# Kernel tuning notes

Hardware: AMD Instinct MI355X
Metric: run time of the kernel (lower is better)

## Reference

```python
import jax, jax.numpy as jnp
import numpy as np

B, S, F = 64, 512, 64
H, L = 512, 4
NH = 8
DH = H // NH
ALPHA = 0.1
EPS = 1e-5


def setup_inputs() -> dict:
    key = jax.random.key(0)
    ks = iter(jax.random.split(key, 40))
    def g(shape, scale=0.05):
        return jax.random.normal(next(ks), shape, dtype=jnp.float32) * scale
    z = lambda *shape: jnp.zeros(shape, dtype=jnp.float32)
    inp = {
        'x': jax.random.normal(next(ks), (B, S, F), dtype=jnp.float32),
        # top-level input projection
        'Win0': g((H, F)), 'bin0': z(H),
        # stacked LTC layer params (L, ...)
        'Wi': g((L, H, H)), 'bi': z(L, H),
        'Wh': g((L, H, H)), 'bh': z(L, H),
        'Wo': g((L, H, H)), 'bo': z(L, H),
        'ln_g': jnp.ones((L, H), dtype=jnp.float32), 'ln_b': z(L, H),
        # multihead self-attention (torch nn.MultiheadAttention packed qkv)
        'in_proj_w': g((3 * H, H)), 'in_proj_b': z(3 * H),
        'out_w': g((H, H)), 'out_b': z(H),
        # direction head
        'Wd1': g((H // 2, H)), 'bd1': z(H // 2),
        'Wd2': g((H // 4, H // 2)), 'bd2': z(H // 4),
        'Wd3': g((2, H // 4)), 'bd3': z(2),
        # price head
        'Wq1': g((H // 2, H)), 'bq1': z(H // 2),
        'Wq2': g((H // 4, H // 2)), 'bq2': z(H // 4),
        'Wq3': g((1, H // 4)), 'bq3': z(1),
        # confidence head
        'Wc1': g((H // 2, H)), 'bc1': z(H // 2),
        'Wc2': g((1, H // 2)), 'bc2': z(1),
    }
    return inp


def _layernorm(x, g, b):
    m = jnp.mean(x, axis=-1, keepdims=True)
    v = jnp.var(x, axis=-1, keepdims=True)
    return (x - m) * jax.lax.rsqrt(v + EPS) * g + b


def _forward(x, Win0, bin0, Wi, bi, Wh, bh, Wo, bo, ln_g, ln_b,
             in_proj_w, in_proj_b, out_w, out_b,
             Wd1, bd1, Wd2, bd2, Wd3, bd3,
             Wq1, bq1, Wq2, bq2, Wq3, bq3,
             Wc1, bc1, Wc2, bc2):
    Bsz = x.shape[0]

    def step(hs, x_t):  # hs: (L, B, H), x_t: (B, F)
        h = x_t @ Win0.T + bin0
        new_hs = []
        for l in range(L):  # fixed small layer count
            comb = h @ Wi[l].T + bi[l] + hs[l] @ Wh[l].T + bh[l]
            nh = hs[l] + ALPHA * (comb - hs[l])  # leaky liquid update
            # torch detaches the carried hidden state (no BPTT)
            new_hs.append(jax.lax.stop_gradient(nh))
            h = _layernorm(nh @ Wo[l].T + bo[l], ln_g[l], ln_b[l])
        return jnp.stack(new_hs), h

    hs0 = jnp.zeros((L, Bsz, H), dtype=x.dtype)
    _, outs = jax.lax.scan(step, hs0, jnp.swapaxes(x, 0, 1))  # (S, B, H)
    seq = jnp.swapaxes(outs, 0, 1)  # (B, S, H)

    # self-attention (eval mode -> no dropout)
    qkv = seq @ in_proj_w.T + in_proj_b
    q, k, v = jnp.split(qkv, 3, axis=-1)
    heads = lambda t: t.reshape(Bsz, -1, NH, DH).transpose(0, 2, 1, 3)
    q, k, v = heads(q), heads(k), heads(v)
    attn = jax.nn.softmax(jnp.einsum('bhqd,bhkd->bhqk', q, k) / np.sqrt(DH).astype(np.float32), axis=-1)
    ao = jnp.einsum('bhqk,bhkd->bhqd', attn, v).transpose(0, 2, 1, 3).reshape(Bsz, -1, H)
    ao = ao @ out_w.T + out_b

    pooled = jnp.mean(seq + ao, axis=1)  # (B, H)

    d = jax.nn.relu(pooled @ Wd1.T + bd1)
    d = jax.nn.relu(d @ Wd2.T + bd2)
    direction_logits = d @ Wd3.T + bd3

    p = jax.nn.relu(pooled @ Wq1.T + bq1)
    p = jax.nn.relu(p @ Wq2.T + bq2)
    price_target = p @ Wq3.T + bq3

    c = jax.nn.relu(pooled @ Wc1.T + bc1)
    confidence = jax.nn.sigmoid(c @ Wc2.T + bc2)

    return direction_logits, price_target, confidence


def reference(x, Win0, bin0, Wi, bi, Wh, bh, Wo, bo, ln_g, ln_b,
              in_proj_w, in_proj_b, out_w, out_b,
              Wd1, bd1, Wd2, bd2, Wd3, bd3,
              Wq1, bq1, Wq2, bq2, Wq3, bq3,
              Wc1, bc1, Wc2, bc2):
    return _forward(x, Win0, bin0, Wi, bi, Wh, bh, Wo, bo, ln_g, ln_b,
                    in_proj_w, in_proj_b, out_w, out_b,
                    Wd1, bd1, Wd2, bd2, Wd3, bd3,
                    Wq1, bq1, Wq2, bq2, Wq3, bq3,
                    Wc1, bc1, Wc2, bc2)
```

## Files before the change

### kernel.cpp

```cpp
#include <hip/hip_runtime.h>

constexpr int kB  = 64;
constexpr int kS  = 512;
constexpr int kF  = 64;
constexpr int kH  = 512;
constexpr int kL  = 4;
constexpr int kDH = 64;
constexpr int kC  = 8;
constexpr int kNC = kS / kC;
constexpr int kSC  = 8;
constexpr int kNSC = kNC / kSC;
#define EPS 1e-5f

typedef __attribute__((ext_vector_type(8))) short short8;
typedef __attribute__((ext_vector_type(4))) float f32x4;

__device__ __forceinline__ ushort f2b(float f){
  unsigned u; __builtin_memcpy(&u, &f, 4);
  unsigned r = (u + 0x7fffu + ((u >> 16) & 1u)) >> 16;
  return (ushort)r;
}
__device__ __forceinline__ float b2f(ushort u){
  unsigned v = ((unsigned)u) << 16; float f; __builtin_memcpy(&f, &v, 4); return f;
}
__device__ __forceinline__ void unpack2(unsigned u, float& a, float& b){
  unsigned lo = u << 16, hi = u & 0xffff0000u;
  __builtin_memcpy(&a, &lo, 4); __builtin_memcpy(&b, &hi, 4);
}

__global__ void cast_scale(const float* __restrict__ src, ushort* __restrict__ dst,
                           int n, float s){
  int i = blockIdx.x*256 + threadIdx.x;
  if (i < n) dst[i] = f2b(src[i]*s);
}

__global__ void zero_f32(float* __restrict__ p, int n){
  int i = blockIdx.x*256 + threadIdx.x;
  if (i < n) p[i] = 0.f;
}

__global__ void prep_afp(const float* __restrict__ Wh, float* __restrict__ Afp){
  int i = blockIdx.x*256 + threadIdx.x;
  if (i >= kL*kH*kH) return;
  const int l = i >> 18, rem = i & 262143;
  const int m = rem >> 9, n = rem & 511;
  float v = b2f(f2b(0.1f * Wh[(size_t)l*kH*kH + (size_t)n*kH + m]));
  if (m == n) v += 0.9f;
  Afp[(size_t)l*kH*kH + (size_t)m*kH + n] = v;
}

__global__ __launch_bounds__(512) void sqgemm(const float* __restrict__ In,
                                              float* __restrict__ Out){
  const int l = blockIdx.x >> 6;
  const int rg = blockIdx.x & 63;
  const int j = threadIdx.x;
  const float* A = In + (size_t)l*kH*kH;
  float* C = Out + (size_t)l*kH*kH;
  __shared__ float ar[8][kH];
  #pragma unroll
  for (int r = 0; r < 8; ++r) ar[r][j] = A[(size_t)(rg*8 + r)*kH + j];
  __syncthreads();
  float acc[8] = {0,0,0,0,0,0,0,0};
  for (int k = 0; k < kH; ++k){
    const float bkj = A[(size_t)k*kH + j];
    #pragma unroll
    for (int r = 0; r < 8; ++r) acc[r] += ar[r][k] * bkj;
  }
  #pragma unroll
  for (int r = 0; r < 8; ++r) C[(size_t)(rg*8 + r)*kH + j] = acc[r];
}

__global__ __launch_bounds__(256) void gemm_bf16(
    const ushort* __restrict__ A, const ushort* __restrict__ W,
    ushort* __restrict__ C, int M, int N, int K,
    const float* __restrict__ pb1, const float* __restrict__ pb2, float bscale)
{
  const int wave = threadIdx.x >> 6, lane = threadIdx.x & 63;
  const int task = blockIdx.x*4 + wave;
  const int NT = N >> 6;
  const int mt = task / NT, ng = task % NT;
  const int r = lane & 15, quad = lane >> 4;

  const ushort* ap = A + (size_t)(mt*64 + r)*K + quad*8;
  const ushort* wp = W + (size_t)(ng*64 + r)*K + quad*8;
  f32x4 acc[4][4];
  #pragma unroll
  for (int t = 0; t < 4; ++t)
    #pragma unroll
    for (int j = 0; j < 4; ++j) acc[t][j] = (f32x4){0,0,0,0};

  for (int k0 = 0; k0 < K; k0 += 32){
    short8 a0 = *(const short8*)(ap + k0);
    short8 a1 = *(const short8*)(ap + (size_t)16*K + k0);
    short8 a2 = *(const short8*)(ap + (size_t)32*K + k0);
    short8 a3 = *(const short8*)(ap + (size_t)48*K + k0);
    short8 b0 = *(const short8*)(wp + k0);
    short8 b1 = *(const short8*)(wp + (size_t)16*K + k0);
    short8 b2 = *(const short8*)(wp + (size_t)32*K + k0);
    short8 b3 = *(const short8*)(wp + (size_t)48*K + k0);
    acc[0][0] = __builtin_amdgcn_mfma_f32_16x16x32_bf16(a0, b0, acc[0][0], 0, 0, 0);
    acc[0][1] = __builtin_amdgcn_mfma_f32_16x16x32_bf16(a0, b1, acc[0][1], 0, 0, 0);
    acc[0][2] = __builtin_amdgcn_mfma_f32_16x16x32_bf16(a0, b2, acc[0][2], 0, 0, 0);
    acc[0][3] = __builtin_amdgcn_mfma_f32_16x16x32_bf16(a0, b3, acc[0][3], 0, 0, 0);
    acc[1][0] = __builtin_amdgcn_mfma_f32_16x16x32_bf16(a1, b0, acc[1][0], 0, 0, 0);
    acc[1][1] = __builtin_amdgcn_mfma_f32_16x16x32_bf16(a1, b1, acc[1][1], 0, 0, 0);
    acc[1][2] = __builtin_amdgcn_mfma_f32_16x16x32_bf16(a1, b2, acc[1][2], 0, 0, 0);
    acc[1][3] = __builtin_amdgcn_mfma_f32_16x16x32_bf16(a1, b3, acc[1][3], 0, 0, 0);
    acc[2][0] = __builtin_amdgcn_mfma_f32_16x16x32_bf16(a2, b0, acc[2][0], 0, 0, 0);
    acc[2][1] = __builtin_amdgcn_mfma_f32_16x16x32_bf16(a2, b1, acc[2][1], 0, 0, 0);
    acc[2][2] = __builtin_amdgcn_mfma_f32_16x16x32_bf16(a2, b2, acc[2][2], 0, 0, 0);
    acc[2][3] = __builtin_amdgcn_mfma_f32_16x16x32_bf16(a2, b3, acc[2][3], 0, 0, 0);
    acc[3][0] = __builtin_amdgcn_mfma_f32_16x16x32_bf16(a3, b0, acc[3][0], 0, 0, 0);
    acc[3][1] = __builtin_amdgcn_mfma_f32_16x16x32_bf16(a3, b1, acc[3][1], 0, 0, 0);
    acc[3][2] = __builtin_amdgcn_mfma_f32_16x16x32_bf16(a3, b2, acc[3][2], 0, 0, 0);
    acc[3][3] = __builtin_amdgcn_mfma_f32_16x16x32_bf16(a3, b3, acc[3][3], 0, 0, 0);
  }
  #pragma unroll
  for (int j = 0; j < 4; ++j){
    const int nn = ng*64 + j*16 + r;
    float bias = 0.f;
    if (pb1) bias += pb1[nn];
    if (pb2) bias += pb2[nn];
    bias *= bscale;
    #pragma unroll
    for (int t = 0; t < 4; ++t){
      #pragma unroll
      for (int i = 0; i < 4; ++i){
        const int mm = mt*64 + t*16 + quad*4 + i;
        C[(size_t)mm*N + nn] = f2b(acc[t][j][i] + bias);
      }
    }
  }
}

template<bool FULL>
__global__ __launch_bounds__(512) void scan_mfma(
    const ushort* __restrict__ U,
    const ushort* __restrict__ G,
    const float* __restrict__ S,
    float* __restrict__ Z,
    ushort* __restrict__ nh)
{
  const int c  = blockIdx.x & (kNC - 1);
  const int b0 = (blockIdx.x / kNC) * 16;
  const int wave = threadIdx.x >> 6, lane = threadIdx.x & 63;
  const int r = lane & 15, quad = lane >> 4;
  const int wbase = wave * 64;
  const int colq = quad * 4;

  __shared__ __align__(16) ushort hiL[2][16*kH];
  __shared__ __align__(16) ushort loL[2][16*kH];

  #define SWZ(row, bytecol) ((row)*1024 + ((bytecol) ^ (((row)&7) << 4)))

  const ushort* gp0 = G + (size_t)(wbase +  0 + r)*kH + quad*8;
  const ushort* gp1 = G + (size_t)(wbase + 16 + r)*kH + quad*8;
  const ushort* gp2 = G + (size_t)(wbase + 32 + r)*kH + quad*8;
  const ushort* gp3 = G + (size_t)(wbase + 48 + r)*kH + quad*8;

  float st[4][4];
  #pragma unroll
  for (int t = 0; t < 4; ++t){
    if (FULL){
      const float4 s4 = *(const float4*)&S[((size_t)(b0 + r)*kNC + c)*kH
                                           + wbase + t*16 + colq];
      st[t][0] = s4.x; st[t][1] = s4.y; st[t][2] = s4.z; st[t][3] = s4.w;
    } else {
      st[t][0] = st[t][1] = st[t][2] = st[t][3] = 0.f;
    }
  }

  #pragma unroll
  for (int t = 0; t < 4; ++t){
    ushort h[4], l[4];
    #pragma unroll
    for (int i = 0; i < 4; ++i){
      h[i] = f2b(st[t][i]);
      l[i] = f2b(st[t][i] - b2f(h[i]));
    }
    uint2 hw, lw;
    hw.x = (unsigned)h[0] | ((unsigned)h[1] << 16);
    hw.y = (unsigned)h[2] | ((unsigned)h[3] << 16);
    lw.x = (unsigned)l[0] | ((unsigned)l[1] << 16);
    lw.y = (unsigned)l[2] | ((unsigned)l[3] << 16);
    const int bc = (wbase + t*16 + colq) * 2;
    *(uint2*)((char*)hiL[0] + SWZ(r, bc)) = hw;
    *(uint2*)((char*)loL[0] + SWZ(r, bc)) = lw;
  }
  __syncthreads();

  const size_t ubase = (size_t)(b0 + r)*kS*kH;
  int cur = 0;

  for (int jj = 0; jj < kC; ++jj){
    const int tt = c*kC + jj;

    uint2 uv[4];
    #pragma unroll
    for (int t = 0; t < 4; ++t)
      uv[t] = *(const uint2*)&U[ubase + (size_t)tt*kH + wbase + t*16 + colq];

    const char* rdHi = (const char*)hiL[cur];
    const char* rdLo = (const char*)loL[cur];
    char* wrHi = (char*)hiL[cur ^ 1];
    char* wrLo = (char*)loL[cur ^ 1];

    f32x4 ah0 = {0,0,0,0}, ah1 = {0,0,0,0}, ah2 = {0,0,0,0}, ah3 = {0,0,0,0};
    f32x4 al0 = {0,0,0,0}, al1 = {0,0,0,0}, al2 = {0,0,0,0}, al3 = {0,0,0,0};
    __builtin_amdgcn_s_setprio(1);
    #pragma unroll 2
    for (int k0 = 0; k0 < kH; k0 += 32){
      const int rb = k0*2 + quad*16;
      const short8 bh = *(const short8*)(rdHi + SWZ(r, rb));
      const short8 bl = *(const short8*)(rdLo + SWZ(r, rb));
      const short8 g0 = *(const short8*)(gp0 + k0);
      const short8 g1 = *(const short8*)(gp1 + k0);
      const short8 g2 = *(const short8*)(gp2 + k0);
      const short8 g3 = *(const short8*)(gp3 + k0);
      ah0 = __builtin_amdgcn_mfma_f32_16x16x32_bf16(g0, bh, ah0, 0, 0, 0);
      ah1 = __builtin_amdgcn_mfma_f32_16x16x32_bf16(g1, bh, ah1, 0, 0, 0);
      ah2 = __builtin_amdgcn_mfma_f32_16x16x32_bf16(g2, bh, ah2, 0, 0, 0);
      ah3 = __builtin_amdgcn_mfma_f32_16x16x32_bf16(g3, bh, ah3, 0, 0, 0);
      al0 = __builtin_amdgcn_mfma_f32_16x16x32_bf16(g0, bl, al0, 0, 0, 0);
      al1 = __builtin_amdgcn_mfma_f32_16x16x32_bf16(g1, bl, al1, 0, 0, 0);
      al2 = __builtin_amdgcn_mfma_f32_16x16x32_bf16(g2, bl, al2, 0, 0, 0);
      al3 = __builtin_amdgcn_mfma_f32_16x16x32_bf16(g3, bl, al3, 0, 0, 0);
    }
    __builtin_amdgcn_s_setprio(0);
    const f32x4 acs[4] = {ah0 + al0, ah1 + al1, ah2 + al2, ah3 + al3};

    #pragma unroll
    for (int t = 0; t < 4; ++t){
      float u0, u1, u2, u3;
      unpack2(uv[t].x, u0, u1); unpack2(uv[t].y, u2, u3);
      const float n0 = 0.9f*st[t][0] + u0 + acs[t][0];
      const float n1 = 0.9f*st[t][1] + u1 + acs[t][1];
      const float n2 = 0.9f*st[t][2] + u2 + acs[t][2];
      const float n3 = 0.9f*st[t][3] + u3 + acs[t][3];
      st[t][0] = n0; st[t][1] = n1; st[t][2] = n2; st[t][3] = n3;
      const ushort h0 = f2b(n0), h1 = f2b(n1), h2 = f2b(n2), h3 = f2b(n3);
      const ushort l0 = f2b(n0 - b2f(h0)), l1 = f2b(n1 - b2f(h1));
      const ushort l2 = f2b(n2 - b2f(h2)), l3 = f2b(n3 - b2f(h3));
      uint2 hw, lw;
      hw.x = (unsigned)h0 | ((unsigned)h1 << 16);
      hw.y = (unsigned)h2 | ((unsigned)h3 << 16);
      lw.x = (unsigned)l0 | ((unsigned)l1 << 16);
      lw.y = (unsigned)l2 | ((unsigned)l3 << 16);
      const int bc = (wbase + t*16 + colq) * 2;
      *(uint2*)(wrHi + SWZ(r, bc)) = hw;
      *(uint2*)(wrLo + SWZ(r, bc)) = lw;
      if (FULL)
        *(uint2*)&nh[ubase + (size_t)tt*kH + wbase + t*16 + colq] = hw;
    }
    __syncthreads();
    cur ^= 1;
  }

  if (!FULL){
    #pragma unroll
    for (int t = 0; t < 4; ++t){
      float4 z4; z4.x = st[t][0]; z4.y = st[t][1]; z4.z = st[t][2]; z4.w = st[t][3];
      *(float4*)&Z[((size_t)(b0 + r)*kNC + c)*kH + wbase + t*16 + colq] = z4;
    }
  }
  #undef SWZ
}

__global__ __launch_bounds__(512) void bscan_a(
    const float* __restrict__ A8, const float* __restrict__ Z,
    float* __restrict__ P8)
{
  const int b = blockIdx.x / kNSC, cc = blockIdx.x % kNSC;
  const int n = threadIdx.x;
  __shared__ float s[kH];
  s[n] = Z[((size_t)b*kNC + cc*kSC)*kH + n];
  __syncthreads();
  for (int j = 1; j < kSC; ++j){
    float acc = Z[((size_t)b*kNC + cc*kSC + j)*kH + n];
    for (int m = 0; m < kH; m += 4){
      const float4 sv = *(const float4*)&s[m];
      acc += sv.x*A8[(size_t)m*kH + n]     + sv.y*A8[(size_t)(m+1)*kH + n]
           + sv.z*A8[(size_t)(m+2)*kH + n] + sv.w*A8[(size_t)(m+3)*kH + n];
    }
    __syncthreads();
    s[n] = acc;
    __syncthreads();
  }
  P8[((size_t)b*kNSC + cc)*kH + n] = s[n];
}

__global__ __launch_bounds__(512) void bscan_b(
    const float* __restrict__ A64, const float* __restrict__ P8,
    float* __restrict__ S2)
{
  const int b = blockIdx.x, n = threadIdx.x;
  __shared__ float s[kH];
  S2[((size_t)b*kNSC + 0)*kH + n] = 0.f;
  s[n] = P8[((size_t)b*kNSC + 0)*kH + n];
  S2[((size_t)b*kNSC + 1)*kH + n] = s[n];
  __syncthreads();
  for (int cc = 1; cc < kNSC - 1; ++cc){
    float acc = P8[((size_t)b*kNSC + cc)*kH + n];
    for (int m = 0; m < kH; m += 4){
      const float4 sv = *(const float4*)&s[m];
      acc += sv.x*A64[(size_t)m*kH + n]     + sv.y*A64[(size_t)(m+1)*kH + n]
           + sv.z*A64[(size_t)(m+2)*kH + n] + sv.w*A64[(size_t)(m+3)*kH + n];
    }
    __syncthreads();
    s[n] = acc;
    S2[((size_t)b*kNSC + cc + 1)*kH + n] = acc;
    __syncthreads();
  }
}

__global__ __launch_bounds__(512) void bscan_c(
    const float* __restrict__ A8, const float* __restrict__ Z,
    const float* __restrict__ S2, float* __restrict__ S)
{
  const int b = blockIdx.x / kNSC, cc = blockIdx.x % kNSC;
  const int n = threadIdx.x;
  __shared__ float s[kH];
  s[n] = S2[((size_t)b*kNSC + cc)*kH + n];
  S[((size_t)b*kNC + cc*kSC)*kH + n] = s[n];
  __syncthreads();
  for (int j = 0; j < kSC - 1; ++j){
    float acc = Z[((size_t)b*kNC + cc*kSC + j)*kH + n];
    for (int m = 0; m < kH; m += 4){
      const float4 sv = *(const float4*)&s[m];
      acc += sv.x*A8[(size_t)m*kH + n]     + sv.y*A8[(size_t)(m+1)*kH + n]
           + sv.z*A8[(size_t)(m+2)*kH + n] + sv.w*A8[(size_t)(m+3)*kH + n];
    }
    __syncthreads();
    s[n] = acc;
    S[((size_t)b*kNC + cc*kSC + j + 1)*kH + n] = acc;
    __syncthreads();
  }
}

__global__ __launch_bounds__(512) void ln_rows(
    ushort* __restrict__ act, const float* __restrict__ g, const float* __restrict__ bta)
{
  const size_t row = blockIdx.x;
  const int n = threadIdx.x, wid = n >> 6, lane = n & 63;
  __shared__ float red[16];
  const float y = b2f(act[row*kH + n]);
  float s1 = y, s2 = y*y;
  #pragma unroll
  for (int off = 32; off; off >>= 1){
    s1 += __shfl_down(s1, off); s2 += __shfl_down(s2, off);
  }
  if (lane == 0){ red[wid] = s1; red[8 + wid] = s2; }
  __syncthreads();
  float m = 0.f, q = 0.f;
  #pragma unroll
  for (int i = 0; i < 8; ++i){ m += red[i]; q += red[8+i]; }
  m *= (1.f/kH); q *= (1.f/kH);
  const float var = q - m*m;
  const float hv = (y - m) * rsqrtf(var + EPS) * g[n] + bta[n];
  act[row*kH + n] = f2b(hv);
}

__global__ __launch_bounds__(512) void seqmean_k(
    const ushort* __restrict__ act, float* __restrict__ seqmean)
{
  const int b = blockIdx.x, n = threadIdx.x;
  float acc = 0.f;
  for (int t = 0; t < kS; ++t) acc += b2f(act[((size_t)b*kS + t)*kH + n]);
  seqmean[(size_t)b*kH + n] = acc * (1.f/kS);
}

__global__ __launch_bounds__(512) void attn_chunk(
    const ushort* __restrict__ qkv,
    float* __restrict__ aomean, int b0)
{
  const int bb = blockIdx.x >> 5;
  const int h  = (blockIdx.x >> 2) & 7;
  const int qt = blockIdx.x & 3;
  const int tid = threadIdx.x, wave = tid >> 6, lane = tid & 63;
  const int r = lane & 15, quad = lane >> 4;

  __shared__ __align__(16) ushort kt[64][72];
  __shared__ __align__(16) ushort vt[64][72];
  __shared__ ushort pt[8][16][72];
  __shared__ float aom[kDH];
  if (tid < kDH) aom[tid] = 0.f;

  const int q0 = qt*128 + wave*16;
  short8 qa0, qa1;
  {
    const ushort* qp = qkv + ((size_t)bb*kS + q0 + r)*(3*kH) + h*kDH + quad*8;
    qa0 = *(const short8*)qp;
    qa1 = *(const short8*)(qp + 32);
  }

  f32x4 oc0={0,0,0,0}, oc1={0,0,0,0}, oc2={0,0,0,0}, oc3={0,0,0,0};
  float mRow[4] = {-1e30f,-1e30f,-1e30f,-1e30f};
  float lRow[4] = {0.f,0.f,0.f,0.f};

  const int srow = tid & 63;
  const int sd0  = (tid >> 6) * 8;

  for (int kt0 = 0; kt0 < kS/64; ++kt0){
    {
      const size_t rbase = ((size_t)bb*kS + kt0*64 + srow)*(3*kH) + h*kDH + sd0;
      *(uint4*)&kt[srow][sd0] = *(const uint4*)(qkv + rbase + kH);
      uint4 v4 = *(const uint4*)(qkv + rbase + 2*kH);
      const ushort* vs = (const ushort*)&v4;
      #pragma unroll
      for (int ii = 0; ii < 8; ++ii) vt[sd0 + ii][srow] = vs[ii];
    }
    __syncthreads();

    f32x4 ac0={0,0,0,0}, ac1={0,0,0,0}, ac2={0,0,0,0}, ac3={0,0,0,0};
    #pragma unroll
    for (int k0 = 0; k0 < 2; ++k0){
      const short8 av = k0 ? qa1 : qa0;
      const short8 b0v = *(const short8*)&kt[ 0 + r][k0*32 + quad*8];
      const short8 b1v = *(const short8*)&kt[16 + r][k0*32 + quad*8];
      const short8 b2v = *(const short8*)&kt[32 + r][k0*32 + quad*8];
      const short8 b3v = *(const short8*)&kt[48 + r][k0*32 + quad*8];
      ac0 = __builtin_amdgcn_mfma_f32_16x16x32_bf16(av, b0v, ac0, 0, 0, 0);
      ac1 = __builtin_amdgcn_mfma_f32_16x16x32_bf16(av, b1v, ac1, 0, 0, 0);
      ac2 = __builtin_amdgcn_mfma_f32_16x16x32_bf16(av, b2v, ac2, 0, 0, 0);
      ac3 = __builtin_amdgcn_mfma_f32_16x16x32_bf16(av, b3v, ac3, 0, 0, 0);
    }
    const f32x4 sc0 = ac0 * 0.125f, sc1 = ac1 * 0.125f,
                sc2 = ac2 * 0.125f, sc3 = ac3 * 0.125f;

    float p0[4], p1[4], p2[4], p3[4];
    #pragma unroll
    for (int i = 0; i < 4; ++i){
      float mx = fmaxf(fmaxf(sc0[i], sc1[i]), fmaxf(sc2[i], sc3[i]));
      #pragma unroll
      for (int off = 1; off < 16; off <<= 1) mx = fmaxf(mx, __shfl_xor(mx, off));
      const float nm = fmaxf(mRow[i], mx);
      const float corr = __expf(mRow[i] - nm);
      mRow[i] = nm;
      p0[i] = __expf(sc0[i] - nm); p1[i] = __expf(sc1[i] - nm);
      p2[i] = __expf(sc2[i] - nm); p3[i] = __expf(sc3[i] - nm);
      float rs = p0[i] + p1[i] + p2[i] + p3[i];
      #pragma unroll
      for (int off = 1; off < 16; off <<= 1) rs += __shfl_xor(rs, off);
      lRow[i] = lRow[i]*corr + rs;
      oc0[i] *= corr; oc1[i] *= corr; oc2[i] *= corr; oc3[i] *= corr;
    }

    #pragma unroll
    for (int i = 0; i < 4; ++i){
      pt[wave][quad*4 + i][ 0 + r] = f2b(p0[i]);
      pt[wave][quad*4 + i][16 + r] = f2b(p1[i]);
      pt[wave][quad*4 + i][32 + r] = f2b(p2[i]);
      pt[wave][quad*4 + i][48 + r] = f2b(p3[i]);
    }

    #pragma unroll
    for (int k0 = 0; k0 < 2; ++k0){
      const short8 pa  = *(const short8*)&pt[wave][r][k0*32 + quad*8];
      const short8 v0v = *(const short8*)&vt[ 0 + r][k0*32 + quad*8];
      const short8 v1v = *(const short8*)&vt[16 + r][k0*32 + quad*8];
      const short8 v2v = *(const short8*)&vt[32 + r][k0*32 + quad*8];
      const short8 v3v = *(const short8*)&vt[48 + r][k0*32 + quad*8];
      oc0 = __builtin_amdgcn_mfma_f32_16x16x32_bf16(pa, v0v, oc0, 0, 0, 0);
      oc1 = __builtin_amdgcn_mfma_f32_16x16x32_bf16(pa, v1v, oc1, 0, 0, 0);
      oc2 = __builtin_amdgcn_mfma_f32_16x16x32_bf16(pa, v2v, oc2, 0, 0, 0);
      oc3 = __builtin_amdgcn_mfma_f32_16x16x32_bf16(pa, v3v, oc3, 0, 0, 0);
    }
    __syncthreads();
  }

  float inv[4];
  #pragma unroll
  for (int i = 0; i < 4; ++i) inv[i] = 1.f / lRow[i];
  {
    float v;
    v = oc0[0]*inv[0] + oc0[1]*inv[1] + oc0[2]*inv[2] + oc0[3]*inv[3];
    v += __shfl_xor(v, 16); v += __shfl_xor(v, 32);
    if (quad == 0) atomicAdd(&aom[ 0 + r], v);
    v = oc1[0]*inv[0] + oc1[1]*inv[1] + oc1[2]*inv[2] + oc1[3]*inv[3];
    v += __shfl_xor(v, 16); v += __shfl_xor(v, 32);
    if (quad == 0) atomicAdd(&aom[16 + r], v);
    v = oc2[0]*inv[0] + oc2[1]*inv[1] + oc2[2]*inv[2] + oc2[3]*inv[3];
    v += __shfl_xor(v, 16); v += __shfl_xor(v, 32);
    if (quad == 0) atomicAdd(&aom[32 + r], v);
    v = oc3[0]*inv[0] + oc3[1]*inv[1] + oc3[2]*inv[2] + oc3[3]*inv[3];
    v += __shfl_xor(v, 16); v += __shfl_xor(v, 32);
    if (quad == 0) atomicAdd(&aom[48 + r], v);
  }
  __syncthreads();
  if (tid < kDH)
    atomicAdd(&aomean[(size_t)(b0 + bb)*kH + h*kDH + tid], aom[tid] * (1.f/kS));
}

__global__ __launch_bounds__(512) void pooled_kernel(
    const float* __restrict__ seqmean, const float* __restrict__ aomean,
    const float* __restrict__ outw, const float* __restrict__ outb,
    float* __restrict__ pooled)
{
  const int b = blockIdx.x, n = threadIdx.x;
  __shared__ float a[kH];
  a[n] = aomean[(size_t)b*kH + n];
  __syncthreads();
  const float* w = outw + (size_t)n*kH;
  float acc = outb[n];
  for (int m = 0; m < kH; ++m) acc += w[m] * a[m];
  pooled[(size_t)b*kH + n] = seqmean[(size_t)b*kH + n] + acc;
}

__global__ __launch_bounds__(256) void heads_kernel(
    const float* __restrict__ pooled,
    const float* Wd1, const float* bd1, const float* Wd2, const float* bd2,
    const float* Wd3, const float* bd3,
    const float* Wq1, const float* bq1, const float* Wq2, const float* bq2,
    const float* Wq3, const float* bq3,
    const float* Wc1, const float* bc1, const float* Wc2, const float* bc2,
    float* __restrict__ out)
{
  const int b = blockIdx.x, tid = threadIdx.x;
  __shared__ float p[kH];
  __shared__ float a1d[256], a1q[256], a1c[256];
  __shared__ float a2d[128], a2q[128];
  p[tid]       = pooled[(size_t)b*kH + tid];
  p[tid + 256] = pooled[(size_t)b*kH + tid + 256];
  __syncthreads();
  {
    const float *w1 = Wd1 + (size_t)tid*kH, *w2 = Wq1 + (size_t)tid*kH,
                *w3 = Wc1 + (size_t)tid*kH;
    float v1 = bd1[tid], v2 = bq1[tid], v3 = bc1[tid];
    for (int m = 0; m < kH; ++m){
      v1 += w1[m]*p[m]; v2 += w2[m]*p[m]; v3 += w3[m]*p[m];
    }
    a1d[tid] = fmaxf(v1, 0.f); a1q[tid] = fmaxf(v2, 0.f); a1c[tid] = fmaxf(v3, 0.f);
  }
  __syncthreads();
  if (tid < 128){
    const float *w1 = Wd2 + (size_t)tid*256, *w2 = Wq2 + (size_t)tid*256;
    float v1 = bd2[tid], v2 = bq2[tid];
    for (int m = 0; m < 256; ++m){ v1 += w1[m]*a1d[m]; v2 += w2[m]*a1q[m]; }
    a2d[tid] = fmaxf(v1, 0.f); a2q[tid] = fmaxf(v2, 0.f);
  }
  __syncthreads();
  if (tid == 0){
    float d0 = bd3[0], d1 = bd3[1], pr = bq3[0], c = bc2[0];
    for (int m = 0; m < 128; ++m){
      d0 += Wd3[m]*a2d[m]; d1 += Wd3[128+m]*a2d[m]; pr += Wq3[m]*a2q[m];
    }
    for (int m = 0; m < 256; ++m) c += Wc2[m]*a1c[m];
    c = 1.f / (1.f + __expf(-c));
    out[2*b + 0]  = d0;
    out[2*b + 1]  = d1;
    out[2*kB + b] = pr;
    out[3*kB + b] = c;
  }
}

extern "C" void kernel_launch(void* const* d_in, const int* in_sizes, int n_in,
                              void* d_out, int out_size, void* d_ws, size_t ws_size,
                              hipStream_t stream) {
  const float* x    = (const float*)d_in[0];
  const float* Win0 = (const float*)d_in[1];
  const float* bin0 = (const float*)d_in[2];
  const float* Wi   = (const float*)d_in[3];
  const float* bi   = (const float*)d_in[4];
  const float* Wh   = (const float*)d_in[5];
  const float* bh   = (const float*)d_in[6];
  const float* Wo   = (const float*)d_in[7];
  const float* bo   = (const float*)d_in[8];
  const float* lng  = (const float*)d_in[9];
  const float* lnb  = (const float*)d_in[10];
  const float* ipw  = (const float*)d_in[11];
  const float* ipb  = (const float*)d_in[12];
  const float* outw = (const float*)d_in[13];
  const float* outb = (const float*)d_in[14];

  char* wsb = (char*)d_ws;
  const size_t MB = 1u << 20;
  ushort* act   = (ushort*)(wsb);
  ushort* U     = (ushort*)(wsb + 32*MB);
  ushort* nh    = (ushort*)(wsb + 64*MB);
  ushort* wh_bf = (ushort*)(wsb + 96*MB);
  ushort* wi_bf = (ushort*)(wsb + 98*MB);
  ushort* wo_bf = (ushort*)(wsb + 100*MB);
  float*  Afp   = (float*)(wsb + 102*MB);
  float*  Afp2  = (float*)(wsb + 106*MB);
  ushort* w0_bf = (ushort*)(wsb + 114*MB);
  ushort* ip_bf = (ushort*)(wsb + 114*MB + 65536);
  ushort* x_bf  = (ushort*)(wsb + 114*MB + 65536 + 1572864);
  float*  Apow  = (float*)x_bf;
  float*  Zb    = (float*)act;
  float*  S     = (float*)(wsb + 8*MB);
  float*  P8    = (float*)(wsb + 16*MB);
  float*  S2    = (float*)(wsb + 17*MB);
  char*   tail  = wsb + 114*MB + 65536 + 1572864 + 4194304;
  float* seqmean = (float*)tail;
  float* aomean  = seqmean + (size_t)kB*kH;
  float* pooled  = aomean  + (size_t)kB*kH;
  ushort* qkv    = U;

  cast_scale<<<(kB*kS*kF + 255)/256, 256, 0, stream>>>(x, x_bf, kB*kS*kF, 1.f);
  cast_scale<<<(kH*kF + 255)/256, 256, 0, stream>>>(Win0, w0_bf, kH*kF, 1.f);
  cast_scale<<<(kL*kH*kH + 255)/256, 256, 0, stream>>>(Wi, wi_bf, kL*kH*kH, 0.1f);
  cast_scale<<<(kL*kH*kH + 255)/256, 256, 0, stream>>>(Wo, wo_bf, kL*kH*kH, 1.f);
  cast_scale<<<(kL*kH*kH + 255)/256, 256, 0, stream>>>(Wh, wh_bf, kL*kH*kH, 0.1f);
  cast_scale<<<(3*kH*kH + 255)/256, 256, 0, stream>>>(ipw, ip_bf, 3*kH*kH, 1.f);
  prep_afp<<<(kL*kH*kH + 255)/256, 256, 0, stream>>>(Wh, Afp);
  sqgemm<<<kL*64, 512, 0, stream>>>(Afp,  Afp2);
  sqgemm<<<kL*64, 512, 0, stream>>>(Afp2, Afp);
  sqgemm<<<kL*64, 512, 0, stream>>>(Afp,  Afp2);

  constexpr int M = kB*kS;
  gemm_bf16<<<(M/64)*(kH/64)/4, 256, 0, stream>>>(x_bf, w0_bf, act, M, kH, kF,
                                                  bin0, nullptr, 1.f);
  sqgemm<<<kL*64, 512, 0, stream>>>(Afp2, Afp);
  sqgemm<<<kL*64, 512, 0, stream>>>(Afp,  Apow);
  sqgemm<<<kL*64, 512, 0, stream>>>(Apow, Afp);

  for (int l = 0; l < kL; ++l){
    gemm_bf16<<<(M/64)*(kH/64)/4, 256, 0, stream>>>(
        act, wi_bf + (size_t)l*kH*kH, U, M, kH, kH,
        bi + (size_t)l*kH, bh + (size_t)l*kH, 0.1f);
    scan_mfma<false><<<4*kNC, 512, 0, stream>>>(U, wh_bf + (size_t)l*kH*kH,
                                                nullptr, Zb, nullptr);
    bscan_a<<<kB*kNSC, 512, 0, stream>>>(Afp2 + (size_t)l*kH*kH, Zb, P8);
    bscan_b<<<kB, 512, 0, stream>>>(Afp + (size_t)l*kH*kH, P8, S2);
    bscan_c<<<kB*kNSC, 512, 0, stream>>>(Afp2 + (size_t)l*kH*kH, Zb, S2, S);
    scan_mfma<true><<<4*kNC, 512, 0, stream>>>(U, wh_bf + (size_t)l*kH*kH,
                                               S, nullptr, nh);
    gemm_bf16<<<(M/64)*(kH/64)/4, 256, 0, stream>>>(
        nh, wo_bf + (size_t)l*kH*kH, act, M, kH, kH,
        bo + (size_t)l*kH, nullptr, 1.f);
    ln_rows<<<M, kH, 0, stream>>>(act, lng + (size_t)l*kH, lnb + (size_t)l*kH);
  }

  seqmean_k<<<kB, kH, 0, stream>>>(act, seqmean);

  zero_f32<<<(kB*kH + 255)/256, 256, 0, stream>>>(aomean, kB*kH);
  for (int c = 0; c < 4; ++c){
    const int Mc = 16*kS;
    gemm_bf16<<<(Mc/64)*(3*kH/64)/4, 256, 0, stream>>>(
        act + (size_t)c*Mc*kH, ip_bf, qkv, Mc, 3*kH, kH, ipb, nullptr, 1.f);
    attn_chunk<<<512, 512, 0, stream>>>(qkv, aomean, c*16);
  }

  pooled_kernel<<<kB, kH, 0, stream>>>(seqmean, aomean, outw, outb, pooled);

  heads_kernel<<<kB, 256, 0, stream>>>(pooled,
      (const float*)d_in[15], (const float*)d_in[16], (const float*)d_in[17],
      (const float*)d_in[18], (const float*)d_in[19], (const float*)d_in[20],
      (const float*)d_in[21], (const float*)d_in[22], (const float*)d_in[23],
      (const float*)d_in[24], (const float*)d_in[25], (const float*)d_in[26],
      (const float*)d_in[27], (const float*)d_in[28], (const float*)d_in[29],
      (const float*)d_in[30], (float*)d_out);
}
```

Measured before the change: 3.667 ms.

## Shorten scan chunks, batch 32 rows per scan block, add hierarchical carry scan

The chunked linear-recurrence scan now uses 4-step chunks (128 chunks) instead of 8, so each block runs a shorter serial chain. Each scan block handles 32 batch rows instead of 16, which reuses the streamed Wh tiles across twice as many rows and keeps the grid at 256 blocks. The single serial carry-propagation kernel is replaced by a three-level hierarchy (h1/h2/h3) using matrix powers A^4, A^32 and A^128, which cuts the serial chain length in the carry pass. In exchange there are more small carry kernels, more squarings of the matrix powers, doubled LDS and register use per scan block, and workspace buffers are reassigned, including P8 aliased onto nh.

Result: slower. 4.278 ms (+16.7%).

```diff
diff --git a/kernel.cpp b/kernel.cpp
--- a/kernel.cpp
+++ b/kernel.cpp
@@ -6,10 +6,12 @@
 constexpr int kH  = 512;
 constexpr int kL  = 4;
 constexpr int kDH = 64;
-constexpr int kC  = 8;
-constexpr int kNC = kS / kC;
+constexpr int kC   = 4;
+constexpr int kNC  = 128;
 constexpr int kSC  = 8;
-constexpr int kNSC = kNC / kSC;
+constexpr int kNSC = 16;
+constexpr int kHC  = 4;
+constexpr int kNHC = 4;
 #define EPS 1e-5f
 
 typedef __attribute__((ext_vector_type(8))) short short8;
@@ -89,6 +91,7 @@
     #pragma unroll
     for (int j = 0; j < 4; ++j) acc[t][j] = (f32x4){0,0,0,0};
 
+  #pragma unroll 2
   for (int k0 = 0; k0 < K; k0 += 32){
     short8 a0 = *(const short8*)(ap + k0);
     short8 a1 = *(const short8*)(ap + (size_t)16*K + k0);
@@ -142,14 +145,14 @@
     ushort* __restrict__ nh)
 {
   const int c  = blockIdx.x & (kNC - 1);
-  const int b0 = (blockIdx.x / kNC) * 16;
+  const int b0 = (blockIdx.x >> 7) * 32;
   const int wave = threadIdx.x >> 6, lane = threadIdx.x & 63;
   const int r = lane & 15, quad = lane >> 4;
   const int wbase = wave * 64;
   const int colq = quad * 4;
 
-  __shared__ __align__(16) ushort hiL[2][16*kH];
-  __shared__ __align__(16) ushort loL[2][16*kH];
+  __shared__ __align__(16) ushort hiL[2][32*kH];
+  __shared__ __align__(16) ushort loL[2][32*kH];
 
   #define SWZ(row, bytecol) ((row)*1024 + ((bytecol) ^ (((row)&7) << 4)))
 
@@ -158,99 +161,126 @@
   const ushort* gp2 = G + (size_t)(wbase + 32 + r)*kH + quad*8;
   const ushort* gp3 = G + (size_t)(wbase + 48 + r)*kH + quad*8;
 
-  float st[4][4];
-  #pragma unroll
-  for (int t = 0; t < 4; ++t){
-    if (FULL){
-      const float4 s4 = *(const float4*)&S[((size_t)(b0 + r)*kNC + c)*kH
-                                           + wbase + t*16 + colq];
-      st[t][0] = s4.x; st[t][1] = s4.y; st[t][2] = s4.z; st[t][3] = s4.w;
-    } else {
-      st[t][0] = st[t][1] = st[t][2] = st[t][3] = 0.f;
-    }
-  }
-
-  #pragma unroll
-  for (int t = 0; t < 4; ++t){
-    ushort h[4], l[4];
-    #pragma unroll
-    for (int i = 0; i < 4; ++i){
-      h[i] = f2b(st[t][i]);
-      l[i] = f2b(st[t][i] - b2f(h[i]));
-    }
-    uint2 hw, lw;
-    hw.x = (unsigned)h[0] | ((unsigned)h[1] << 16);
-    hw.y = (unsigned)h[2] | ((unsigned)h[3] << 16);
-    lw.x = (unsigned)l[0] | ((unsigned)l[1] << 16);
-    lw.y = (unsigned)l[2] | ((unsigned)l[3] << 16);
-    const int bc = (wbase + t*16 + colq) * 2;
-    *(uint2*)((char*)hiL[0] + SWZ(r, bc)) = hw;
-    *(uint2*)((char*)loL[0] + SWZ(r, bc)) = lw;
-  }
-  __syncthreads();
-
-  const size_t ubase = (size_t)(b0 + r)*kS*kH;
+  float st[2][4][4];
+  #pragma unroll
+  for (int bt = 0; bt < 2; ++bt)
+    #pragma unroll
+    for (int t = 0; t < 4; ++t){
+      if (FULL){
+        const float4 s4 = *(const float4*)&S[((size_t)(b0 + bt*16 + r)*kNC + c)*kH
+                                             + wbase + t*16 + colq];
+        st[bt][t][0] = s4.x; st[bt][t][1] = s4.y;
+        st[bt][t][2] = s4.z; st[bt][t][3] = s4.w;
+      } else {
+        st[bt][t][0] = st[bt][t][1] = st[bt][t][2] = st[bt][t][3] = 0.f;
+      }
+    }
+
+  #pragma unroll
+  for (int bt = 0; bt < 2; ++bt)
+    #pragma unroll
+    for (int t = 0; t < 4; ++t){
+      ushort h[4], l[4];
+      #pragma unroll
+      for (int i = 0; i < 4; ++i){
+        h[i] = f2b(st[bt][t][i]);
+        l[i] = f2b(st[bt][t][i] - b2f(h[i]));
+      }
+      uint2 hw, lw;
+      hw.x = (unsigned)h[0] | ((unsigned)h[1] << 16);
+      hw.y = (unsigned)h[2] | ((unsigned)h[3] << 16);
+      lw.x = (unsigned)l[0] | ((unsigned)l[1] << 16);
+      lw.y = (unsigned)l[2] | ((unsigned)l[3] << 16);
+      const int bc = (wbase + t*16 + colq) * 2;
+      *(uint2*)((char*)hiL[0] + SWZ(bt*16 + r, bc)) = hw;
+      *(uint2*)((char*)loL[0] + SWZ(bt*16 + r, bc)) = lw;
+    }
+  __syncthreads();
+
+  const size_t ub0 = (size_t)(b0 +  0 + r)*kS*kH;
+  const size_t ub1 = (size_t)(b0 + 16 + r)*kS*kH;
   int cur = 0;
 
   for (int jj = 0; jj < kC; ++jj){
     const int tt = c*kC + jj;
 
-    uint2 uv[4];
-    #pragma unroll
-    for (int t = 0; t < 4; ++t)
-      uv[t] = *(const uint2*)&U[ubase + (size_t)tt*kH + wbase + t*16 + colq];
+    uint2 uv[2][4];
+    #pragma unroll
+    for (int t = 0; t < 4; ++t){
+      uv[0][t] = *(const uint2*)&U[ub0 + (size_t)tt*kH + wbase + t*16 + colq];
+      uv[1][t] = *(const uint2*)&U[ub1 + (size_t)tt*kH + wbase + t*16 + colq];
+    }
 
     const char* rdHi = (const char*)hiL[cur];
     const char* rdLo = (const char*)loL[cur];
     char* wrHi = (char*)hiL[cur ^ 1];
     char* wrLo = (char*)loL[cur ^ 1];
 
-    f32x4 ah0 = {0,0,0,0}, ah1 = {0,0,0,0}, ah2 = {0,0,0,0}, ah3 = {0,0,0,0};
-    f32x4 al0 = {0,0,0,0}, al1 = {0,0,0,0}, al2 = {0,0,0,0}, al3 = {0,0,0,0};
+    f32x4 ah[2][4], al[2][4];
+    #pragma unroll
+    for (int bt = 0; bt < 2; ++bt)
+      #pragma unroll
+      for (int t = 0; t < 4; ++t){ ah[bt][t] = (f32x4){0,0,0,0}; al[bt][t] = (f32x4){0,0,0,0}; }
+
     __builtin_amdgcn_s_setprio(1);
     #pragma unroll 2
     for (int k0 = 0; k0 < kH; k0 += 32){
       const int rb = k0*2 + quad*16;
-      const short8 bh = *(const short8*)(rdHi + SWZ(r, rb));
-      const short8 bl = *(const short8*)(rdLo + SWZ(r, rb));
+      const short8 bh0 = *(const short8*)(rdHi + SWZ( 0 + r, rb));
+      const short8 bl0 = *(const short8*)(rdLo + SWZ( 0 + r, rb));
+      const short8 bh1 = *(const short8*)(rdHi + SWZ(16 + r, rb));
+      const short8 bl1 = *(const short8*)(rdLo + SWZ(16 + r, rb));
       const short8 g0 = *(const short8*)(gp0 + k0);
       const short8 g1 = *(const short8*)(gp1 + k0);
       const short8 g2 = *(const short8*)(gp2 + k0);
       const short8 g3 = *(const short8*)(gp3 + k0);
-      ah0 = __builtin_amdgcn_mfma_f32_16x16x32_bf16(g0, bh, ah0, 0, 0, 0);
-      ah1 = __builtin_amdgcn_mfma_f32_16x16x32_bf16(g1, bh, ah1, 0, 0, 0);
-      ah2 = __builtin_amdgcn_mfma_f32_16x16x32_bf16(g2, bh, ah2, 0, 0, 0);
-      ah3 = __builtin_amdgcn_mfma_f32_16x16x32_bf16(g3, bh, ah3, 0, 0, 0);
-      al0 = __builtin_amdgcn_mfma_f32_16x16x32_bf16(g0, bl, al0, 0, 0, 0);
-      al1 = __builtin_amdgcn_mfma_f32_16x16x32_bf16(g1, bl, al1, 0, 0, 0);
-      al2 = __builtin_amdgcn_mfma_f32_16x16x32_bf16(g2, bl, al2, 0, 0, 0);
-      al3 = __builtin_amdgcn_mfma_f32_16x16x32_bf16(g3, bl, al3, 0, 0, 0);
+      ah[0][0] = __builtin_amdgcn_mfma_f32_16x16x32_bf16(g0, bh0, ah[0][0], 0, 0, 0);
+      ah[0][1] = __builtin_amdgcn_mfma_f32_16x16x32_bf16(g1, bh0, ah[0][1], 0, 0, 0);
+      ah[0][2] = __builtin_amdgcn_mfma_f32_16x16x32_bf16(g2, bh0, ah[0][2], 0, 0, 0);
+      ah[0][3] = __builtin_amdgcn_mfma_f32_16x16x32_bf16(g3, bh0, ah[0][3], 0, 0, 0);
+      al[0][0] = __builtin_amdgcn_mfma_f32_16x16x32_bf16(g0, bl0, al[0][0], 0, 0, 0);
+      al[0][1] = __builtin_amdgcn_mfma_f32_16x16x32_bf16(g1, bl0, al[0][1], 0, 0, 0);
+      al[0][2] = __builtin_amdgcn_mfma_f32_16x16x32_bf16(g2, bl0, al[0][2], 0, 0, 0);
+      al[0][3] = __builtin_amdgcn_mfma_f32_16x16x32_bf16(g3, bl0, al[0][3], 0, 0, 0);
+      ah[1][0] = __builtin_amdgcn_mfma_f32_16x16x32_bf16(g0, bh1, ah[1][0], 0, 0, 0);
+      ah[1][1] = __builtin_amdgcn_mfma_f32_16x16x32_bf16(g1, bh1, ah[1][1], 0, 0, 0);
+      ah[1][2] = __builtin_amdgcn_mfma_f32_16x16x32_bf16(g2, bh1, ah[1][2], 0, 0, 0);
+      ah[1][3] = __builtin_amdgcn_mfma_f32_16x16x32_bf16(g3, bh1, ah[1][3], 0, 0, 0);
+      al[1][0] = __builtin_amdgcn_mfma_f32_16x16x32_bf16(g0, bl1, al[1][0], 0, 0, 0);
+      al[1][1] = __builtin_amdgcn_mfma_f32_16x16x32_bf16(g1, bl1, al[1][1], 0, 0, 0);
+      al[1][2] = __builtin_amdgcn_mfma_f32_16x16x32_bf16(g2, bl1, al[1][2], 0, 0, 0);
+      al[1][3] = __builtin_amdgcn_mfma_f32_16x16x32_bf16(g3, bl1, al[1][3], 0, 0, 0);
     }
     __builtin_amdgcn_s_setprio(0);
-    const f32x4 acs[4] = {ah0 + al0, ah1 + al1, ah2 + al2, ah3 + al3};
-
-    #pragma unroll
-    for (int t = 0; t < 4; ++t){
-      float u0, u1, u2, u3;
-      unpack2(uv[t].x, u0, u1); unpack2(uv[t].y, u2, u3);
-      const float n0 = 0.9f*st[t][0] + u0 + acs[t][0];
-      const float n1 = 0.9f*st[t][1] + u1 + acs[t][1];
-      const float n2 = 0.9f*st[t][2] + u2 + acs[t][2];
-      const float n3 = 0.9f*st[t][3] + u3 + acs[t][3];
-      st[t][0] = n0; st[t][1] = n1; st[t][2] = n2; st[t][3] = n3;
-      const ushort h0 = f2b(n0), h1 = f2b(n1), h2 = f2b(n2), h3 = f2b(n3);
-      const ushort l0 = f2b(n0 - b2f(h0)), l1 = f2b(n1 - b2f(h1));
-      const ushort l2 = f2b(n2 - b2f(h2)), l3 = f2b(n3 - b2f(h3));
-      uint2 hw, lw;
-      hw.x = (unsigned)h0 | ((unsigned)h1 << 16);
-      hw.y = (unsigned)h2 | ((unsigned)h3 << 16);
-      lw.x = (unsigned)l0 | ((unsigned)l1 << 16);
-      lw.y = (unsigned)l2 | ((unsigned)l3 << 16);
-      const int bc = (wbase + t*16 + colq) * 2;
-      *(uint2*)(wrHi + SWZ(r, bc)) = hw;
-      *(uint2*)(wrLo + SWZ(r, bc)) = lw;
-      if (FULL)
-        *(uint2*)&nh[ubase + (size_t)tt*kH + wbase + t*16 + colq] = hw;
+
+    #pragma unroll
+    for (int bt = 0; bt < 2; ++bt){
+      const size_t ub = bt ? ub1 : ub0;
+      #pragma unroll
+      for (int t = 0; t < 4; ++t){
+        const f32x4 acs = ah[bt][t] + al[bt][t];
+        float u0, u1, u2, u3;
+        unpack2(uv[bt][t].x, u0, u1); unpack2(uv[bt][t].y, u2, u3);
+        const float n0 = 0.9f*st[bt][t][0] + u0 + acs[0];
+        const float n1 = 0.9f*st[bt][t][1] + u1 + acs[1];
+        const float n2 = 0.9f*st[bt][t][2] + u2 + acs[2];
+        const float n3 = 0.9f*st[bt][t][3] + u3 + acs[3];
+        st[bt][t][0] = n0; st[bt][t][1] = n1;
+        st[bt][t][2] = n2; st[bt][t][3] = n3;
+        const ushort h0 = f2b(n0), h1 = f2b(n1), h2 = f2b(n2), h3 = f2b(n3);
+        const ushort l0 = f2b(n0 - b2f(h0)), l1 = f2b(n1 - b2f(h1));
+        const ushort l2 = f2b(n2 - b2f(h2)), l3 = f2b(n3 - b2f(h3));
+        uint2 hw, lw;
+        hw.x = (unsigned)h0 | ((unsigned)h1 << 16);
+        hw.y = (unsigned)h2 | ((unsigned)h3 << 16);
+        lw.x = (unsigned)l0 | ((unsigned)l1 << 16);
+        lw.y = (unsigned)l2 | ((unsigned)l3 << 16);
+        const int bc = (wbase + t*16 + colq) * 2;
+        *(uint2*)(wrHi + SWZ(bt*16 + r, bc)) = hw;
+        *(uint2*)(wrLo + SWZ(bt*16 + r, bc)) = lw;
+        if (FULL)
+          *(uint2*)&nh[ub + (size_t)tt*kH + wbase + t*16 + colq] = hw;
+      }
     }
     __syncthreads();
     cur ^= 1;
@@ -258,16 +288,21 @@
 
   if (!FULL){
     #pragma unroll
-    for (int t = 0; t < 4; ++t){
-      float4 z4; z4.x = st[t][0]; z4.y = st[t][1]; z4.z = st[t][2]; z4.w = st[t][3];
-      *(float4*)&Z[((size_t)(b0 + r)*kNC + c)*kH + wbase + t*16 + colq] = z4;
-    }
+    for (int bt = 0; bt < 2; ++bt)
+      #pragma unroll
+      for (int t = 0; t < 4; ++t){
+        float4 z4; z4.x = st[bt][t][0]; z4.y = st[bt][t][1];
+        z4.z = st[bt][t][2]; z4.w = st[bt][t][3];
+        *(float4*)&Z[((size_t)(b0 + bt*16 + r)*kNC + c)*kH
+                     + wbase + t*16 + colq] = z4;
+      }
   }
   #undef SWZ
 }
 
+
 __global__ __launch_bounds__(512) void bscan_a(
-    const float* __restrict__ A8, const float* __restrict__ Z,
+    const float* __restrict__ A4, const float* __restrict__ Z,
     float* __restrict__ P8)
 {
   const int b = blockIdx.x / kNSC, cc = blockIdx.x % kNSC;
@@ -279,8 +314,8 @@
     float acc = Z[((size_t)b*kNC + cc*kSC + j)*kH + n];
     for (int m = 0; m < kH; m += 4){
       const float4 sv = *(const float4*)&s[m];
-      acc += sv.x*A8[(size_t)m*kH + n]     + sv.y*A8[(size_t)(m+1)*kH + n]
-           + sv.z*A8[(size_t)(m+2)*kH + n] + sv.w*A8[(size_t)(m+3)*kH + n];
+      acc += sv.x*A4[(size_t)m*kH + n]     + sv.y*A4[(size_t)(m+1)*kH + n]
+           + sv.z*A4[(size_t)(m+2)*kH + n] + sv.w*A4[(size_t)(m+3)*kH + n];
     }
     __syncthreads();
     s[n] = acc;
@@ -289,32 +324,79 @@
   P8[((size_t)b*kNSC + cc)*kH + n] = s[n];
 }
 
-__global__ __launch_bounds__(512) void bscan_b(
-    const float* __restrict__ A64, const float* __restrict__ P8,
-    float* __restrict__ S2)
+__global__ __launch_bounds__(512) void bscan_h1(
+    const float* __restrict__ A32, const float* __restrict__ P8,
+    float* __restrict__ Ph)
+{
+  const int b = blockIdx.x / kNHC, hc = blockIdx.x % kNHC;
+  const int n = threadIdx.x;
+  __shared__ float s[kH];
+  s[n] = P8[((size_t)b*kNSC + hc*kHC)*kH + n];
+  __syncthreads();
+  for (int j = 1; j < kHC; ++j){
+    float acc = P8[((size_t)b*kNSC + hc*kHC + j)*kH + n];
+    for (int m = 0; m < kH; m += 4){
+      const float4 sv = *(const float4*)&s[m];
+      acc += sv.x*A32[(size_t)m*kH + n]     + sv.y*A32[(size_t)(m+1)*kH + n]
+           + sv.z*A32[(size_t)(m+2)*kH + n] + sv.w*A32[(size_t)(m+3)*kH + n];
+    }
+    __syncthreads();
+    s[n] = acc;
+    __syncthreads();
+  }
+  Ph[((size_t)b*kNHC + hc)*kH + n] = s[n];
+}
+
+__global__ __launch_bounds__(512) void bscan_h2(
+    const float* __restrict__ A128, const float* __restrict__ Ph,
+    float* __restrict__ Sh)
 {
   const int b = blockIdx.x, n = threadIdx.x;
   __shared__ float s[kH];
-  S2[((size_t)b*kNSC + 0)*kH + n] = 0.f;
-  s[n] = P8[((size_t)b*kNSC + 0)*kH + n];
-  S2[((size_t)b*kNSC + 1)*kH + n] = s[n];
-  __syncthreads();
-  for (int cc = 1; cc < kNSC - 1; ++cc){
-    float acc = P8[((size_t)b*kNSC + cc)*kH + n];
+  Sh[((size_t)b*kNHC + 0)*kH + n] = 0.f;
+  s[n] = Ph[((size_t)b*kNHC + 0)*kH + n];
+  Sh[((size_t)b*kNHC + 1)*kH + n] = s[n];
+  __syncthreads();
+  for (int hc = 1; hc < kNHC - 1; ++hc){
+    float acc = Ph[((size_t)b*kNHC + hc)*kH + n];
     for (int m = 0; m < kH; m += 4){
       const float4 sv = *(const float4*)&s[m];
-      acc += sv.x*A64[(size_t)m*kH + n]     + sv.y*A64[(size_t)(m+1)*kH + n]
-           + sv.z*A64[(size_t)(m+2)*kH + n] + sv.w*A64[(size_t)(m+3)*kH + n];
+      acc += sv.x*A128[(size_t)m*kH + n]     + sv.y*A128[(size_t)(m+1)*kH + n]
+           + sv.z*A128[(size_t)(m+2)*kH + n] + sv.w*A128[(size_t)(m+3)*kH + n];
     }
     __syncthreads();
     s[n] = acc;
-    S2[((size_t)b*kNSC + cc + 1)*kH + n] = acc;
+    Sh[((size_t)b*kNHC + hc + 1)*kH + n] = acc;
+    __syncthreads();
+  }
+}
+
+__global__ __launch_bounds__(512) void bscan_h3(
+    const float* __restrict__ A32, const float* __restrict__ P8,
+    const float* __restrict__ Sh, float* __restrict__ S2)
+{
+  const int b = blockIdx.x / kNHC, hc = blockIdx.x % kNHC;
+  const int n = threadIdx.x;
+  __shared__ float s[kH];
+  s[n] = Sh[((size_t)b*kNHC + hc)*kH + n];
+  S2[((size_t)b*kNSC + hc*kHC)*kH + n] = s[n];
+  __syncthreads();
+  for (int j = 0; j < kHC - 1; ++j){
+    float acc = P8[((size_t)b*kNSC + hc*kHC + j)*kH + n];
+    for (int m = 0; m < kH; m += 4){
+      const float4 sv = *(const float4*)&s[m];
+      acc += sv.x*A32[(size_t)m*kH + n]     + sv.y*A32[(size_t)(m+1)*kH + n]
+           + sv.z*A32[(size_t)(m+2)*kH + n] + sv.w*A32[(size_t)(m+3)*kH + n];
+    }
+    __syncthreads();
+    s[n] = acc;
+    S2[((size_t)b*kNSC + hc*kHC + j + 1)*kH + n] = acc;
     __syncthreads();
   }
 }
 
 __global__ __launch_bounds__(512) void bscan_c(
-    const float* __restrict__ A8, const float* __restrict__ Z,
+    const float* __restrict__ A4, const float* __restrict__ Z,
     const float* __restrict__ S2, float* __restrict__ S)
 {
   const int b = blockIdx.x / kNSC, cc = blockIdx.x % kNSC;
@@ -327,8 +409,8 @@
     float acc = Z[((size_t)b*kNC + cc*kSC + j)*kH + n];
     for (int m = 0; m < kH; m += 4){
       const float4 sv = *(const float4*)&s[m];
-      acc += sv.x*A8[(size_t)m*kH + n]     + sv.y*A8[(size_t)(m+1)*kH + n]
-           + sv.z*A8[(size_t)(m+2)*kH + n] + sv.w*A8[(size_t)(m+3)*kH + n];
+      acc += sv.x*A4[(size_t)m*kH + n]     + sv.y*A4[(size_t)(m+1)*kH + n]
+           + sv.z*A4[(size_t)(m+2)*kH + n] + sv.w*A4[(size_t)(m+3)*kH + n];
     }
     __syncthreads();
     s[n] = acc;
@@ -582,14 +664,17 @@
   ushort* wo_bf = (ushort*)(wsb + 100*MB);
   float*  Afp   = (float*)(wsb + 102*MB);
   float*  Afp2  = (float*)(wsb + 106*MB);
+  float*  A128b = (float*)(wsb + 110*MB);
   ushort* w0_bf = (ushort*)(wsb + 114*MB);
   ushort* ip_bf = (ushort*)(wsb + 114*MB + 65536);
   ushort* x_bf  = (ushort*)(wsb + 114*MB + 65536 + 1572864);
   float*  Apow  = (float*)x_bf;
   float*  Zb    = (float*)act;
-  float*  S     = (float*)(wsb + 8*MB);
-  float*  P8    = (float*)(wsb + 16*MB);
-  float*  S2    = (float*)(wsb + 17*MB);
+  float*  S     = (float*)(wsb + 16*MB);
+  float*  P8    = (float*)nh;
+  float*  S2    = (float*)(wsb + 66*MB);
+  float*  Ph    = (float*)(wsb + 68*MB);
+  float*  Sh    = (float*)(wsb + 69*MB);
   char*   tail  = wsb + 114*MB + 65536 + 1572864 + 4194304;
   float* seqmean = (float*)tail;
   float* aomean  = seqmean + (size_t)kB*kH;
@@ -605,25 +690,28 @@
   prep_afp<<<(kL*kH*kH + 255)/256, 256, 0, stream>>>(Wh, Afp);
   sqgemm<<<kL*64, 512, 0, stream>>>(Afp,  Afp2);
   sqgemm<<<kL*64, 512, 0, stream>>>(Afp2, Afp);
-  sqgemm<<<kL*64, 512, 0, stream>>>(Afp,  Afp2);
 
   constexpr int M = kB*kS;
   gemm_bf16<<<(M/64)*(kH/64)/4, 256, 0, stream>>>(x_bf, w0_bf, act, M, kH, kF,
                                                   bin0, nullptr, 1.f);
-  sqgemm<<<kL*64, 512, 0, stream>>>(Afp2, Afp);
-  sqgemm<<<kL*64, 512, 0, stream>>>(Afp,  Apow);
-  sqgemm<<<kL*64, 512, 0, stream>>>(Apow, Afp);
+  sqgemm<<<kL*64, 512, 0, stream>>>(Afp,  Afp2);
+  sqgemm<<<kL*64, 512, 0, stream>>>(Afp2, Apow);
+  sqgemm<<<kL*64, 512, 0, stream>>>(Apow, Afp2);
+  sqgemm<<<kL*64, 512, 0, stream>>>(Afp2, Apow);
+  sqgemm<<<kL*64, 512, 0, stream>>>(Apow, A128b);
 
   for (int l = 0; l < kL; ++l){
     gemm_bf16<<<(M/64)*(kH/64)/4, 256, 0, stream>>>(
         act, wi_bf + (size_t)l*kH*kH, U, M, kH, kH,
         bi + (size_t)l*kH, bh + (size_t)l*kH, 0.1f);
-    scan_mfma<false><<<4*kNC, 512, 0, stream>>>(U, wh_bf + (size_t)l*kH*kH,
+    scan_mfma<false><<<2*kNC, 512, 0, stream>>>(U, wh_bf + (size_t)l*kH*kH,
                                                 nullptr, Zb, nullptr);
-    bscan_a<<<kB*kNSC, 512, 0, stream>>>(Afp2 + (size_t)l*kH*kH, Zb, P8);
-    bscan_b<<<kB, 512, 0, stream>>>(Afp + (size_t)l*kH*kH, P8, S2);
-    bscan_c<<<kB*kNSC, 512, 0, stream>>>(Afp2 + (size_t)l*kH*kH, Zb, S2, S);
-    scan_mfma<true><<<4*kNC, 512, 0, stream>>>(U, wh_bf + (size_t)l*kH*kH,
+    bscan_a<<<kB*kNSC, 512, 0, stream>>>(Afp + (size_t)l*kH*kH, Zb, P8);
+    bscan_h1<<<kB*kNHC, 512, 0, stream>>>(Afp2 + (size_t)l*kH*kH, P8, Ph);
+    bscan_h2<<<kB, 512, 0, stream>>>(A128b + (size_t)l*kH*kH, Ph, Sh);
+    bscan_h3<<<kB*kNHC, 512, 0, stream>>>(Afp2 + (size_t)l*kH*kH, P8, Sh, S2);
+    bscan_c<<<kB*kNSC, 512, 0, stream>>>(Afp + (size_t)l*kH*kH, Zb, S2, S);
+    scan_mfma<true><<<2*kNC, 512, 0, stream>>>(U, wh_bf + (size_t)l*kH*kH,
                                                S, nullptr, nh);
     gemm_bf16<<<(M/64)*(kH/64)/4, 256, 0, stream>>>(
         nh, wo_bf + (size_t)l*kH*kH, act, M, kH, kH,
```
